# Kernel tuning notes

Measured on AMD Instinct MI355X. Metric: run time of the kernel, lower is better.

## Reference

```python
import jax, jax.numpy as jnp
import numpy as np

N_NODES = 100000
N_EDGES = 1600000
D_IN = 128
D_OUT = 128
N_RATES = 5


def setup_inputs() -> dict:
    key = jax.random.key(0)
    k1, k2, k3, k4, k5 = jax.random.split(key, 5)
    h = jax.random.normal(k1, (N_NODES, D_IN), dtype=jnp.float32)
    W = jax.random.normal(k2, (N_RATES, D_IN, D_OUT), dtype=jnp.float32) / np.sqrt(D_IN)
    b = jnp.zeros((N_RATES, D_OUT), dtype=jnp.float32)
    src = jax.random.randint(k3, (N_EDGES,), 0, N_NODES, dtype=jnp.int64)
    dst = jax.random.randint(k4, (N_EDGES,), 0, N_NODES, dtype=jnp.int64)
    rate = jax.random.randint(k5, (N_EDGES,), 0, N_RATES, dtype=jnp.int64)
    return {"h": h, "W": W, "b": b, "src": src, "dst": dst, "rate": rate}


def reference(h, W, b, src, dst, rate):
    # Per-rate edge-masked GraphConv (dgl GraphConv, norm='both'), outputs concatenated.
    # Edge subgraph is expressed as a 0/1 edge weight so shapes stay static under jit.
    N = h.shape[0]
    outs = []
    for r in range(W.shape[0]):  # small fixed set of relation types
        w_e = (rate == r).astype(h.dtype)                      # [E] subgraph mask
        out_deg = jax.ops.segment_sum(w_e, src, num_segments=N)
        in_deg = jax.ops.segment_sum(w_e, dst, num_segments=N)
        norm_src = jnp.maximum(out_deg, 1.0) ** -0.5           # dgl clamps deg to >=1
        norm_dst = jnp.maximum(in_deg, 1.0) ** -0.5
        feat = h * norm_src[:, None]                           # D_out^{-1/2} h
        msg = feat[src] * w_e[:, None]                         # gather + mask [E, D]
        agg = jax.ops.segment_sum(msg, dst, num_segments=N)    # SpMM aggregation
        outs.append((agg @ W[r]) * norm_dst[:, None] + b[r])   # weight, D_in^{-1/2}, bias
    return jnp.concatenate(outs, axis=1)                       # [N, N_RATES*D_OUT]
```

## Files before the change

kernel.cpp:

```cpp
#include <hip/hip_runtime.h>

#define N_NODES 100000
#define N_EDGES 1600000
#define DIM 128
#define N_RATES 5
#define OUT_W (N_RATES * DIM)
#define PK_SHIFT 17
#define PK_MASK  0x1FFFF
#define SCAN_NB ((N_NODES + 1023) / 1024)

#define WS_DEG_OUT 0x000000u
#define WS_DEG_IN  0x200000u
#define WS_NSRC    0x400000u
#define WS_NDST    0x600000u
#define WS_OFFS    0x800000u
#define WS_CURSOR  0x880000u
#define WS_BSUM    0x900000u
#define WS_PACKED  0xA00000u
#define WS_G       0x1100000u
#define SLOT_BYTES ((size_t)N_NODES * DIM * sizeof(float))

__global__ __launch_bounds__(256) void deg_kernel(const int* __restrict__ src,
                                                  const int* __restrict__ dst,
                                                  const int* __restrict__ rate,
                                                  int* __restrict__ deg_out,
                                                  int* __restrict__ deg_in) {
    int e = blockIdx.x * 256 + threadIdx.x;
    if (e >= N_EDGES) return;
    int r = rate[e];
    atomicAdd(&deg_out[r * N_NODES + src[e]], 1);
    atomicAdd(&deg_in [r * N_NODES + dst[e]], 1);
}

__global__ __launch_bounds__(256) void norm_kernel(const int* __restrict__ deg_out,
                                                   const int* __restrict__ deg_in,
                                                   float* __restrict__ nsrc,
                                                   float* __restrict__ ndst) {
    int i = blockIdx.x * 256 + threadIdx.x;
    if (i >= N_RATES * N_NODES) return;
    int d0 = deg_out[i]; if (d0 < 1) d0 = 1;
    int d1 = deg_in[i];  if (d1 < 1) d1 = 1;
    nsrc[i] = 1.0f / sqrtf((float)d0);
    ndst[i] = 1.0f / sqrtf((float)d1);
}

__global__ __launch_bounds__(256) void scan1_kernel(const int* __restrict__ deg_in,
                                                    int* __restrict__ offs,
                                                    int* __restrict__ bsum) {
    __shared__ int sh[256];
    int tid = threadIdx.x;
    int base = blockIdx.x * 1024 + tid * 4;
    int v[4];
#pragma unroll
    for (int j = 0; j < 4; ++j) {
        int idx = base + j, s = 0;
        if (idx < N_NODES) {
#pragma unroll
            for (int r = 0; r < N_RATES; ++r) s += deg_in[r * N_NODES + idx];
        }
        v[j] = s;
    }
    int tsum = v[0] + v[1] + v[2] + v[3];
    sh[tid] = tsum;
    __syncthreads();
    for (int off = 1; off < 256; off <<= 1) {
        int t = (tid >= off) ? sh[tid - off] : 0;
        __syncthreads();
        sh[tid] += t;
        __syncthreads();
    }
    int excl = sh[tid] - tsum;
#pragma unroll
    for (int j = 0; j < 4; ++j) {
        int idx = base + j;
        if (idx < N_NODES) offs[idx] = excl;
        excl += v[j];
    }
    if (tid == 255) bsum[blockIdx.x] = sh[255];
}

__global__ void scan2_kernel(int* __restrict__ bsum) {
    if (threadIdx.x != 0 || blockIdx.x != 0) return;
    int run = 0;
    for (int i = 0; i < SCAN_NB; ++i) { int t = bsum[i]; bsum[i] = run; run += t; }
}

__global__ __launch_bounds__(256) void scan3_kernel(int* __restrict__ offs,
                                                    const int* __restrict__ bsum,
                                                    int* __restrict__ cursor) {
    int i = blockIdx.x * 256 + threadIdx.x;
    if (i >= N_NODES) return;
    int v = offs[i] + bsum[i >> 10];
    offs[i] = v;
    cursor[i] = v;
}

__global__ __launch_bounds__(256) void fill_kernel(const int* __restrict__ src,
                                                   const int* __restrict__ dst,
                                                   const int* __restrict__ rate,
                                                   int* __restrict__ cursor,
                                                   int* __restrict__ packed) {
    int e = blockIdx.x * 256 + threadIdx.x;
    if (e >= N_EDGES) return;
    int pos = atomicAdd(&cursor[dst[e]], 1);
    packed[pos] = src[e] | (rate[e] << PK_SHIFT);
}

__global__ __launch_bounds__(256) void gemm_g_kernel(const float* __restrict__ h,
                                                     const float* __restrict__ Wall,
                                                     const float* __restrict__ nsrc,
                                                     float* __restrict__ G,
                                                     int rbase) {
    __shared__ float sW[32][128];
    __shared__ float sA[32][64];
    int slot = blockIdx.y;
    int r = rbase + slot;
    const float* W  = Wall + (size_t)r * DIM * DIM;
    const float* ns = nsrc + (size_t)r * N_NODES;
    int tid  = threadIdx.x;
    int row0 = blockIdx.x * 64;
    int c2   = (tid & 63) * 2;
    int rg   = tid >> 6;
    int rb   = rg * 16;

    float acc0[16], acc1[16];
#pragma unroll
    for (int i = 0; i < 16; ++i) { acc0[i] = 0.f; acc1[i] = 0.f; }

    for (int kc = 0; kc < 128; kc += 32) {
        __syncthreads();
#pragma unroll
        for (int j = 0; j < 4; ++j) {
            int f = tid * 4 + j * 1024;
            int kl = f >> 7, c = f & 127;
            *(float4*)(&sW[kl][c]) = *(const float4*)(W + (kc + kl) * 128 + c);
        }
#pragma unroll
        for (int j = 0; j < 2; ++j) {
            int f = tid * 4 + j * 1024;
            int rowl = f >> 5, kl = f & 31;
            int grow = row0 + rowl;
            float4 a4 = make_float4(0.f, 0.f, 0.f, 0.f);
            if (grow < N_NODES) a4 = *(const float4*)(h + (size_t)grow * DIM + kc + kl);
            sA[kl + 0][rowl] = a4.x; sA[kl + 1][rowl] = a4.y;
            sA[kl + 2][rowl] = a4.z; sA[kl + 3][rowl] = a4.w;
        }
        __syncthreads();
#pragma unroll
        for (int k = 0; k < 32; ++k) {
            float2 w = *(const float2*)(&sW[k][c2]);
#pragma unroll
            for (int i = 0; i < 4; ++i) {
                float4 a = *(const float4*)(&sA[k][rb + i * 4]);
                acc0[i*4+0] += a.x * w.x; acc1[i*4+0] += a.x * w.y;
                acc0[i*4+1] += a.y * w.x; acc1[i*4+1] += a.y * w.y;
                acc0[i*4+2] += a.z * w.x; acc1[i*4+2] += a.z * w.y;
                acc0[i*4+3] += a.w * w.x; acc1[i*4+3] += a.w * w.y;
            }
        }
    }
#pragma unroll
    for (int i = 0; i < 16; ++i) {
        int row = row0 + rb + i;
        if (row < N_NODES) {
            float nsv = ns[row];
            float2 o; o.x = acc0[i] * nsv; o.y = acc1[i] * nsv;
            *(float2*)(G + ((size_t)slot * N_NODES + row) * DIM + c2) = o;
        }
    }
}

template<int GS, bool ALL>
__global__ __launch_bounds__(256) void gather_kernel(const float* __restrict__ G,
                                                     const int* __restrict__ packed,
                                                     const int* __restrict__ offs,
                                                     const float* __restrict__ ndst,
                                                     const float* __restrict__ bias,
                                                     float* __restrict__ out,
                                                     int rbase) {
    int gw   = (blockIdx.x * 256 + threadIdx.x) >> 6;
    int lane = threadIdx.x & 63;
    if (gw >= N_NODES) return;
    int d = gw;
    int beg = offs[d];
    int end = (d == N_NODES - 1) ? N_EDGES : offs[d + 1];

    float2 a0 = make_float2(0.f, 0.f), a1 = a0, a2 = a0, a3 = a0, a4 = a0;

    int p = beg;
    for (; p + 4 <= end; p += 4) {
        int pk[4]; int rl[4]; bool use[4]; float2 v[4];
#pragma unroll
        for (int i = 0; i < 4; ++i) pk[i] = packed[p + i];
#pragma unroll
        for (int i = 0; i < 4; ++i) {
            rl[i]  = (pk[i] >> PK_SHIFT) - rbase;
            use[i] = ALL || ((unsigned)rl[i] < (unsigned)GS);
        }
#pragma unroll
        for (int i = 0; i < 4; ++i) {
            int s = pk[i] & PK_MASK;
            if (use[i])
                v[i] = *(const float2*)(G + ((size_t)rl[i] * N_NODES + s) * DIM + lane * 2);
        }
#pragma unroll
        for (int i = 0; i < 4; ++i) {
            if (!use[i]) continue;
            switch (rl[i]) {
                case 0: a0.x += v[i].x; a0.y += v[i].y; break;
                case 1: if constexpr (GS > 1) { a1.x += v[i].x; a1.y += v[i].y; } break;
                case 2: if constexpr (GS > 2) { a2.x += v[i].x; a2.y += v[i].y; } break;
                case 3: if constexpr (GS > 3) { a3.x += v[i].x; a3.y += v[i].y; } break;
                default: if constexpr (GS > 4) { a4.x += v[i].x; a4.y += v[i].y; } break;
            }
        }
    }
    for (; p < end; ++p) {
        int pkx = packed[p];
        int rlx = (pkx >> PK_SHIFT) - rbase;
        if (!ALL && (unsigned)rlx >= (unsigned)GS) continue;
        int s = pkx & PK_MASK;
        float2 v = *(const float2*)(G + ((size_t)rlx * N_NODES + s) * DIM + lane * 2);
        switch (rlx) {
            case 0: a0.x += v.x; a0.y += v.y; break;
            case 1: if constexpr (GS > 1) { a1.x += v.x; a1.y += v.y; } break;
            case 2: if constexpr (GS > 2) { a2.x += v.x; a2.y += v.y; } break;
            case 3: if constexpr (GS > 3) { a3.x += v.x; a3.y += v.y; } break;
            default: if constexpr (GS > 4) { a4.x += v.x; a4.y += v.y; } break;
        }
    }

    float* orow = out + (size_t)d * OUT_W + lane * 2;
#pragma unroll
    for (int ri = 0; ri < GS; ++ri) {
        int r = rbase + ri;
        float ndv = ndst[(size_t)r * N_NODES + d];
        float2 bb = *(const float2*)(bias + r * DIM + lane * 2);
        float2 acc = (ri == 0) ? a0 : (ri == 1) ? a1 : (ri == 2) ? a2
                   : (ri == 3) ? a3 : a4;
        float2 o; o.x = acc.x * ndv + bb.x; o.y = acc.y * ndv + bb.y;
        *(float2*)(orow + r * DIM) = o;
    }
}

__global__ __launch_bounds__(256) void zero_out_kernel(float4* __restrict__ out) {
    int i = blockIdx.x * 256 + threadIdx.x;
    if (i < N_NODES * OUT_W / 4) out[i] = make_float4(0.f, 0.f, 0.f, 0.f);
}

__global__ __launch_bounds__(256) void scatter_c_kernel(const float* __restrict__ h,
                                                        const int* __restrict__ src,
                                                        const int* __restrict__ dst,
                                                        const int* __restrict__ rate,
                                                        const float* __restrict__ nsrc,
                                                        float* __restrict__ out) {
    int lane = threadIdx.x & 63;
    int gw = (blockIdx.x * 256 + threadIdx.x) >> 6;
    int e0 = gw * 4;
#pragma unroll
    for (int i = 0; i < 4; ++i) {
        int e = e0 + i;
        if (e >= N_EDGES) return;
        int s = src[e], d = dst[e], r = rate[e];
        float ns = nsrc[(size_t)r * N_NODES + s];
        float2 v = *(const float2*)(h + (size_t)s * DIM + lane * 2);
        float* o = out + (size_t)d * OUT_W + r * DIM + lane * 2;
        unsafeAtomicAdd(o,     v.x * ns);
        unsafeAtomicAdd(o + 1, v.y * ns);
    }
}

__global__ __launch_bounds__(256) void gemm_inplace_kernel(float* __restrict__ outp,
                                                           const float* __restrict__ Wall,
                                                           const float* __restrict__ bias,
                                                           const float* __restrict__ ndst,
                                                           int r) {
    __shared__ float sW[32][128];
    __shared__ float sA[32][64];
    float* A = outp + r * DIM;
    const float* Wr = Wall + (size_t)r * DIM * DIM;
    const float* nd = ndst + (size_t)r * N_NODES;
    const float* br = bias + (size_t)r * DIM;
    int tid  = threadIdx.x;
    int row0 = blockIdx.x * 64;
    int c2   = (tid & 63) * 2;
    int rg   = tid >> 6;
    int rb   = rg * 16;
    float acc0[16], acc1[16];
#pragma unroll
    for (int i = 0; i < 16; ++i) { acc0[i] = 0.f; acc1[i] = 0.f; }
    for (int kc = 0; kc < 128; kc += 32) {
        __syncthreads();
#pragma unroll
        for (int j = 0; j < 4; ++j) {
            int f = tid * 4 + j * 1024;
            int kl = f >> 7, c = f & 127;
            *(float4*)(&sW[kl][c]) = *(const float4*)(Wr + (kc + kl) * 128 + c);
        }
#pragma unroll
        for (int j = 0; j < 2; ++j) {
            int f = tid * 4 + j * 1024;
            int rowl = f >> 5, kl = f & 31;
            int grow = row0 + rowl;
            float4 a4 = make_float4(0.f, 0.f, 0.f, 0.f);
            if (grow < N_NODES) a4 = *(const float4*)(A + (size_t)grow * OUT_W + kc + kl);
            sA[kl + 0][rowl] = a4.x; sA[kl + 1][rowl] = a4.y;
            sA[kl + 2][rowl] = a4.z; sA[kl + 3][rowl] = a4.w;
        }
        __syncthreads();
#pragma unroll
        for (int k = 0; k < 32; ++k) {
            float2 w = *(const float2*)(&sW[k][c2]);
#pragma unroll
            for (int i = 0; i < 4; ++i) {
                float4 a = *(const float4*)(&sA[k][rb + i * 4]);
                acc0[i*4+0] += a.x * w.x; acc1[i*4+0] += a.x * w.y;
                acc0[i*4+1] += a.y * w.x; acc1[i*4+1] += a.y * w.y;
                acc0[i*4+2] += a.z * w.x; acc1[i*4+2] += a.z * w.y;
                acc0[i*4+3] += a.w * w.x; acc1[i*4+3] += a.w * w.y;
            }
        }
    }
#pragma unroll
    for (int i = 0; i < 16; ++i) {
        int row = row0 + rb + i;
        if (row < N_NODES) {
            float ndv = nd[row];
            float2 o;
            o.x = acc0[i] * ndv + br[c2];
            o.y = acc1[i] * ndv + br[c2 + 1];
            *(float2*)(A + (size_t)row * OUT_W + c2) = o;
        }
    }
}

extern "C" void kernel_launch(void* const* d_in, const int* in_sizes, int n_in,
                              void* d_out, int out_size, void* d_ws, size_t ws_size,
                              hipStream_t stream) {
    const float* h    = (const float*)d_in[0];
    const float* W    = (const float*)d_in[1];
    const float* b    = (const float*)d_in[2];
    const int*   src  = (const int*)d_in[3];
    const int*   dst  = (const int*)d_in[4];
    const int*   rate = (const int*)d_in[5];
    float* out = (float*)d_out;

    char* ws = (char*)d_ws;
    int*   deg_out = (int*)(ws + WS_DEG_OUT);
    int*   deg_in  = (int*)(ws + WS_DEG_IN);
    float* nsrc    = (float*)(ws + WS_NSRC);
    float* ndst    = (float*)(ws + WS_NDST);
    int*   offs    = (int*)(ws + WS_OFFS);
    int*   cursor  = (int*)(ws + WS_CURSOR);
    int*   bsum    = (int*)(ws + WS_BSUM);
    int*   packed  = (int*)(ws + WS_PACKED);
    float* G       = (float*)(ws + WS_G);

    int n_slots = 0;
    if (ws_size > WS_G) n_slots = (int)((ws_size - WS_G) / SLOT_BYTES);
    if (n_slots > N_RATES) n_slots = N_RATES;

    hipMemsetAsync(ws, 0, 0x400000, stream);
    deg_kernel<<<(N_EDGES + 255) / 256, 256, 0, stream>>>(src, dst, rate, deg_out, deg_in);
    norm_kernel<<<(N_RATES * N_NODES + 255) / 256, 256, 0, stream>>>(deg_out, deg_in,
                                                                     nsrc, ndst);

    if (n_slots >= 1) {
        scan1_kernel<<<SCAN_NB, 256, 0, stream>>>(deg_in, offs, bsum);
        scan2_kernel<<<1, 1, 0, stream>>>(bsum);
        scan3_kernel<<<(N_NODES + 255) / 256, 256, 0, stream>>>(offs, bsum, cursor);
        fill_kernel<<<(N_EDGES + 255) / 256, 256, 0, stream>>>(src, dst, rate,
                                                               cursor, packed);
        const int ggrid = (N_NODES * 64 + 255) / 256;
        int done = 0;
        while (done < N_RATES) {
            int gs = N_RATES - done; if (gs > n_slots) gs = n_slots;
            gemm_g_kernel<<<dim3((N_NODES + 63) / 64, gs), 256, 0, stream>>>(h, W, nsrc,
                                                                             G, done);
            switch (gs) {
                case 5: gather_kernel<5, true ><<<ggrid, 256, 0, stream>>>(G, packed, offs,
                                                                           ndst, b, out, done); break;
                case 4: gather_kernel<4, false><<<ggrid, 256, 0, stream>>>(G, packed, offs,
                                                                           ndst, b, out, done); break;
                case 3: gather_kernel<3, false><<<ggrid, 256, 0, stream>>>(G, packed, offs,
                                                                           ndst, b, out, done); break;
                case 2: gather_kernel<2, false><<<ggrid, 256, 0, stream>>>(G, packed, offs,
                                                                           ndst, b, out, done); break;
                default: gather_kernel<1, false><<<ggrid, 256, 0, stream>>>(G, packed, offs,
                                                                            ndst, b, out, done); break;
            }
            done += gs;
        }
    } else {
        zero_out_kernel<<<(N_NODES * OUT_W / 4 + 255) / 256, 256, 0, stream>>>((float4*)out);
        scatter_c_kernel<<<(N_EDGES / 4 * 64 + 255) / 256, 256, 0, stream>>>(h, src, dst,
                                                                             rate, nsrc, out);
        for (int r = 0; r < N_RATES; ++r)
            gemm_inplace_kernel<<<(N_NODES + 63) / 64, 256, 0, stream>>>(out, W, b, ndst, r);
    }
}
```

Baseline: 948.1 us.

## Aggregate raw features first, then apply weights with split-bf16 MFMA GEMM

Reorders the computation so the gather aggregates source-normalized h directly, applying nsrc per edge, instead of gathering a precomputed h·W per rate. The per-rate aggregates are stored as hi/lo bf16 pairs and multiplied by W using a new MFMA kernel with three-term split-bf16 products to approximate fp32 accuracy. This removes the large fp32 G materialization. The gather now reads a single shared h table instead of five rate-specific tables, improving cache reuse, at the cost of an extra per-edge nsrc load and a bf16 intermediate round trip.

```diff
diff --git a/kernel.cpp b/kernel.cpp
--- a/kernel.cpp
+++ b/kernel.cpp
@@ -1,4 +1,5 @@
 #include <hip/hip_runtime.h>
+#include <hip/hip_bf16.h>
 
 #define N_NODES 100000
 #define N_EDGES 1600000
@@ -8,6 +9,7 @@
 #define PK_SHIFT 17
 #define PK_MASK  0x1FFFF
 #define SCAN_NB ((N_NODES + 1023) / 1024)
+#define MT_TILES ((N_NODES + 63) / 64)
 
 #define WS_DEG_OUT 0x000000u
 #define WS_DEG_IN  0x200000u
@@ -18,7 +20,10 @@
 #define WS_BSUM    0x900000u
 #define WS_PACKED  0xA00000u
 #define WS_G       0x1100000u
-#define SLOT_BYTES ((size_t)N_NODES * DIM * sizeof(float))
+#define SLOT_BYTES ((size_t)N_NODES * 256 * sizeof(unsigned short))
+
+typedef float f4     __attribute__((ext_vector_type(4)));
+typedef short bf16x8 __attribute__((ext_vector_type(8)));
 
 __global__ __launch_bounds__(256) void deg_kernel(const int* __restrict__ src,
                                                   const int* __restrict__ dst,
@@ -106,82 +111,17 @@
     packed[pos] = src[e] | (rate[e] << PK_SHIFT);
 }
 
-__global__ __launch_bounds__(256) void gemm_g_kernel(const float* __restrict__ h,
-                                                     const float* __restrict__ Wall,
-                                                     const float* __restrict__ nsrc,
-                                                     float* __restrict__ G,
-                                                     int rbase) {
-    __shared__ float sW[32][128];
-    __shared__ float sA[32][64];
-    int slot = blockIdx.y;
-    int r = rbase + slot;
-    const float* W  = Wall + (size_t)r * DIM * DIM;
-    const float* ns = nsrc + (size_t)r * N_NODES;
-    int tid  = threadIdx.x;
-    int row0 = blockIdx.x * 64;
-    int c2   = (tid & 63) * 2;
-    int rg   = tid >> 6;
-    int rb   = rg * 16;
-
-    float acc0[16], acc1[16];
-#pragma unroll
-    for (int i = 0; i < 16; ++i) { acc0[i] = 0.f; acc1[i] = 0.f; }
-
-    for (int kc = 0; kc < 128; kc += 32) {
-        __syncthreads();
-#pragma unroll
-        for (int j = 0; j < 4; ++j) {
-            int f = tid * 4 + j * 1024;
-            int kl = f >> 7, c = f & 127;
-            *(float4*)(&sW[kl][c]) = *(const float4*)(W + (kc + kl) * 128 + c);
-        }
-#pragma unroll
-        for (int j = 0; j < 2; ++j) {
-            int f = tid * 4 + j * 1024;
-            int rowl = f >> 5, kl = f & 31;
-            int grow = row0 + rowl;
-            float4 a4 = make_float4(0.f, 0.f, 0.f, 0.f);
-            if (grow < N_NODES) a4 = *(const float4*)(h + (size_t)grow * DIM + kc + kl);
-            sA[kl + 0][rowl] = a4.x; sA[kl + 1][rowl] = a4.y;
-            sA[kl + 2][rowl] = a4.z; sA[kl + 3][rowl] = a4.w;
-        }
-        __syncthreads();
-#pragma unroll
-        for (int k = 0; k < 32; ++k) {
-            float2 w = *(const float2*)(&sW[k][c2]);
-#pragma unroll
-            for (int i = 0; i < 4; ++i) {
-                float4 a = *(const float4*)(&sA[k][rb + i * 4]);
-                acc0[i*4+0] += a.x * w.x; acc1[i*4+0] += a.x * w.y;
-                acc0[i*4+1] += a.y * w.x; acc1[i*4+1] += a.y * w.y;
-                acc0[i*4+2] += a.z * w.x; acc1[i*4+2] += a.z * w.y;
-                acc0[i*4+3] += a.w * w.x; acc1[i*4+3] += a.w * w.y;
-            }
-        }
-    }
-#pragma unroll
-    for (int i = 0; i < 16; ++i) {
-        int row = row0 + rb + i;
-        if (row < N_NODES) {
-            float nsv = ns[row];
-            float2 o; o.x = acc0[i] * nsv; o.y = acc1[i] * nsv;
-            *(float2*)(G + ((size_t)slot * N_NODES + row) * DIM + c2) = o;
-        }
-    }
-}
-
 template<int GS, bool ALL>
-__global__ __launch_bounds__(256) void gather_kernel(const float* __restrict__ G,
+__global__ __launch_bounds__(256) void gather_kernel(const float* __restrict__ h,
                                                      const int* __restrict__ packed,
                                                      const int* __restrict__ offs,
-                                                     const float* __restrict__ ndst,
-                                                     const float* __restrict__ bias,
-                                                     float* __restrict__ out,
+                                                     const float* __restrict__ nsrc,
+                                                     unsigned short* __restrict__ agg,
                                                      int rbase) {
     int gw   = (blockIdx.x * 256 + threadIdx.x) >> 6;
     int lane = threadIdx.x & 63;
     if (gw >= N_NODES) return;
-    int d = gw;
+    const int d = gw;
     int beg = offs[d];
     int end = (d == N_NODES - 1) ? N_EDGES : offs[d + 1];
 
@@ -189,7 +129,7 @@
 
     int p = beg;
     for (; p + 4 <= end; p += 4) {
-        int pk[4]; int rl[4]; bool use[4]; float2 v[4];
+        int pk[4]; int rl[4]; bool use[4]; float2 v[4]; float ns[4];
 #pragma unroll
         for (int i = 0; i < 4; ++i) pk[i] = packed[p + i];
 #pragma unroll
@@ -200,18 +140,21 @@
 #pragma unroll
         for (int i = 0; i < 4; ++i) {
             int s = pk[i] & PK_MASK;
-            if (use[i])
-                v[i] = *(const float2*)(G + ((size_t)rl[i] * N_NODES + s) * DIM + lane * 2);
+            if (use[i]) {
+                v[i]  = *(const float2*)(h + (size_t)s * DIM + lane * 2);
+                ns[i] = nsrc[(size_t)(rl[i] + rbase) * N_NODES + s];
+            }
         }
 #pragma unroll
         for (int i = 0; i < 4; ++i) {
             if (!use[i]) continue;
+            float tx = v[i].x * ns[i], ty = v[i].y * ns[i];
             switch (rl[i]) {
-                case 0: a0.x += v[i].x; a0.y += v[i].y; break;
-                case 1: if constexpr (GS > 1) { a1.x += v[i].x; a1.y += v[i].y; } break;
-                case 2: if constexpr (GS > 2) { a2.x += v[i].x; a2.y += v[i].y; } break;
-                case 3: if constexpr (GS > 3) { a3.x += v[i].x; a3.y += v[i].y; } break;
-                default: if constexpr (GS > 4) { a4.x += v[i].x; a4.y += v[i].y; } break;
+                case 0: a0.x += tx; a0.y += ty; break;
+                case 1: if constexpr (GS > 1) { a1.x += tx; a1.y += ty; } break;
+                case 2: if constexpr (GS > 2) { a2.x += tx; a2.y += ty; } break;
+                case 3: if constexpr (GS > 3) { a3.x += tx; a3.y += ty; } break;
+                default: if constexpr (GS > 4) { a4.x += tx; a4.y += ty; } break;
             }
         }
     }
@@ -220,26 +163,107 @@
         int rlx = (pkx >> PK_SHIFT) - rbase;
         if (!ALL && (unsigned)rlx >= (unsigned)GS) continue;
         int s = pkx & PK_MASK;
-        float2 v = *(const float2*)(G + ((size_t)rlx * N_NODES + s) * DIM + lane * 2);
+        float2 v = *(const float2*)(h + (size_t)s * DIM + lane * 2);
+        float ns = nsrc[(size_t)(rlx + rbase) * N_NODES + s];
+        float tx = v.x * ns, ty = v.y * ns;
         switch (rlx) {
-            case 0: a0.x += v.x; a0.y += v.y; break;
-            case 1: if constexpr (GS > 1) { a1.x += v.x; a1.y += v.y; } break;
-            case 2: if constexpr (GS > 2) { a2.x += v.x; a2.y += v.y; } break;
-            case 3: if constexpr (GS > 3) { a3.x += v.x; a3.y += v.y; } break;
-            default: if constexpr (GS > 4) { a4.x += v.x; a4.y += v.y; } break;
-        }
-    }
-
-    float* orow = out + (size_t)d * OUT_W + lane * 2;
+            case 0: a0.x += tx; a0.y += ty; break;
+            case 1: if constexpr (GS > 1) { a1.x += tx; a1.y += ty; } break;
+            case 2: if constexpr (GS > 2) { a2.x += tx; a2.y += ty; } break;
+            case 3: if constexpr (GS > 3) { a3.x += tx; a3.y += ty; } break;
+            default: if constexpr (GS > 4) { a4.x += tx; a4.y += ty; } break;
+        }
+    }
+
 #pragma unroll
     for (int ri = 0; ri < GS; ++ri) {
-        int r = rbase + ri;
-        float ndv = ndst[(size_t)r * N_NODES + d];
-        float2 bb = *(const float2*)(bias + r * DIM + lane * 2);
         float2 acc = (ri == 0) ? a0 : (ri == 1) ? a1 : (ri == 2) ? a2
                    : (ri == 3) ? a3 : a4;
-        float2 o; o.x = acc.x * ndv + bb.x; o.y = acc.y * ndv + bb.y;
-        *(float2*)(orow + r * DIM) = o;
+        unsigned short* row = agg + ((size_t)ri * N_NODES + d) * 256;
+        __bf16 hx = (__bf16)acc.x; __bf16 lx = (__bf16)(acc.x - (float)hx);
+        __bf16 hy = (__bf16)acc.y; __bf16 ly = (__bf16)(acc.y - (float)hy);
+        unsigned int hv = (unsigned int)__builtin_bit_cast(unsigned short, hx)
+                        | ((unsigned int)__builtin_bit_cast(unsigned short, hy) << 16);
+        unsigned int lv = (unsigned int)__builtin_bit_cast(unsigned short, lx)
+                        | ((unsigned int)__builtin_bit_cast(unsigned short, ly) << 16);
+        *(unsigned int*)(row + lane * 2)       = hv;
+        *(unsigned int*)(row + 128 + lane * 2) = lv;
+    }
+}
+
+__global__ __launch_bounds__(256) void gemm_agg_kernel(const unsigned short* __restrict__ agg,
+                                                       const float* __restrict__ Wall,
+                                                       const float* __restrict__ bias,
+                                                       const float* __restrict__ ndst,
+                                                       float* __restrict__ out,
+                                                       int rbase) {
+    __shared__ __align__(16) unsigned short sWt[2][128][136];
+    const int slot = blockIdx.y;
+    const int r = rbase + slot;
+    const float* Wr = Wall + (size_t)r * DIM * DIM;
+    const int tid = threadIdx.x;
+
+#pragma unroll
+    for (int phase = 0; phase < 16; ++phase) {
+        int f = phase * 1024 + tid * 4;
+        int k = f >> 7, n = f & 127;
+        float4 w4 = *(const float4*)(Wr + f);
+        float wv[4] = {w4.x, w4.y, w4.z, w4.w};
+#pragma unroll
+        for (int j = 0; j < 4; ++j) {
+            __bf16 hb = (__bf16)wv[j];
+            __bf16 lb = (__bf16)(wv[j] - (float)hb);
+            sWt[0][n + j][k] = __builtin_bit_cast(unsigned short, hb);
+            sWt[1][n + j][k] = __builtin_bit_cast(unsigned short, lb);
+        }
+    }
+    __syncthreads();
+
+    const int w = tid >> 6, l = tid & 63;
+    const int lrow = l & 15;
+    const int lk   = (l >> 4) * 8;
+    const int lq4  = (l >> 4) * 4;
+    const float* ndr = ndst + (size_t)r * N_NODES;
+    const float* br  = bias + (size_t)r * DIM;
+
+    for (int mt = blockIdx.x; mt < MT_TILES; mt += gridDim.x) {
+        int rowA = mt * 64 + w * 16 + lrow;
+        int rowAc = rowA < N_NODES ? rowA : 0;
+        const unsigned short* arow = agg + ((size_t)slot * N_NODES + rowAc) * 256;
+
+        f4 acc[8];
+#pragma unroll
+        for (int i = 0; i < 8; ++i) acc[i] = (f4){0.f, 0.f, 0.f, 0.f};
+
+#pragma unroll
+        for (int ks = 0; ks < 4; ++ks) {
+            int k0 = ks * 32;
+            bf16x8 ah = *(const bf16x8*)(arow + k0 + lk);
+            bf16x8 al = *(const bf16x8*)(arow + 128 + k0 + lk);
+#pragma unroll
+            for (int nt = 0; nt < 8; ++nt) {
+                bf16x8 bh = *(const bf16x8*)&sWt[0][nt * 16 + lrow][k0 + lk];
+                bf16x8 bl = *(const bf16x8*)&sWt[1][nt * 16 + lrow][k0 + lk];
+                acc[nt] = __builtin_amdgcn_mfma_f32_16x16x32_bf16(ah, bh, acc[nt], 0, 0, 0);
+                acc[nt] = __builtin_amdgcn_mfma_f32_16x16x32_bf16(ah, bl, acc[nt], 0, 0, 0);
+                acc[nt] = __builtin_amdgcn_mfma_f32_16x16x32_bf16(al, bh, acc[nt], 0, 0, 0);
+            }
+        }
+
+        int rowD0 = mt * 64 + w * 16 + lq4;
+#pragma unroll
+        for (int q = 0; q < 4; ++q) {
+            int row = rowD0 + q;
+            if (row < N_NODES) {
+                float ndv = ndr[row];
+                float* orow = out + (size_t)row * OUT_W + r * DIM;
+#pragma unroll
+                for (int nt = 0; nt < 8; ++nt) {
+                    int col = nt * 16 + lrow;
+                    orow[col] = acc[nt][q] * ndv + br[col];
+                }
+            }
+        }
     }
 }
 
@@ -310,14 +334,14 @@
         __syncthreads();
 #pragma unroll
         for (int k = 0; k < 32; ++k) {
-            float2 w = *(const float2*)(&sW[k][c2]);
+            float2 wv = *(const float2*)(&sW[k][c2]);
 #pragma unroll
             for (int i = 0; i < 4; ++i) {
                 float4 a = *(const float4*)(&sA[k][rb + i * 4]);
-                acc0[i*4+0] += a.x * w.x; acc1[i*4+0] += a.x * w.y;
-                acc0[i*4+1] += a.y * w.x; acc1[i*4+1] += a.y * w.y;
-                acc0[i*4+2] += a.z * w.x; acc1[i*4+2] += a.z * w.y;
-                acc0[i*4+3] += a.w * w.x; acc1[i*4+3] += a.w * w.y;
+                acc0[i*4+0] += a.x * wv.x; acc1[i*4+0] += a.x * wv.y;
+                acc0[i*4+1] += a.y * wv.x; acc1[i*4+1] += a.y * wv.y;
+                acc0[i*4+2] += a.z * wv.x; acc1[i*4+2] += a.z * wv.y;
+                acc0[i*4+3] += a.w * wv.x; acc1[i*4+3] += a.w * wv.y;
             }
         }
     }
@@ -354,7 +378,7 @@
     int*   cursor  = (int*)(ws + WS_CURSOR);
     int*   bsum    = (int*)(ws + WS_BSUM);
     int*   packed  = (int*)(ws + WS_PACKED);
-    float* G       = (float*)(ws + WS_G);
+    unsigned short* agg = (unsigned short*)(ws + WS_G);
 
     int n_slots = 0;
     if (ws_size > WS_G) n_slots = (int)((ws_size - WS_G) / SLOT_BYTES);
@@ -375,20 +399,19 @@
         int done = 0;
         while (done < N_RATES) {
             int gs = N_RATES - done; if (gs > n_slots) gs = n_slots;
-            gemm_g_kernel<<<dim3((N_NODES + 63) / 64, gs), 256, 0, stream>>>(h, W, nsrc,
-                                                                             G, done);
             switch (gs) {
-                case 5: gather_kernel<5, true ><<<ggrid, 256, 0, stream>>>(G, packed, offs,
-                                                                           ndst, b, out, done); break;
-                case 4: gather_kernel<4, false><<<ggrid, 256, 0, stream>>>(G, packed, offs,
-                                                                           ndst, b, out, done); break;
-                case 3: gather_kernel<3, false><<<ggrid, 256, 0, stream>>>(G, packed, offs,
-                                                                           ndst, b, out, done); break;
-                case 2: gather_kernel<2, false><<<ggrid, 256, 0, stream>>>(G, packed, offs,
-                                                                           ndst, b, out, done); break;
-                default: gather_kernel<1, false><<<ggrid, 256, 0, stream>>>(G, packed, offs,
-                                                                            ndst, b, out, done); break;
-            }
+                case 5: gather_kernel<5, true ><<<ggrid, 256, 0, stream>>>(h, packed, offs,
+                                                                           nsrc, agg, done); break;
+                case 4: gather_kernel<4, false><<<ggrid, 256, 0, stream>>>(h, packed, offs,
+                                                                           nsrc, agg, done); break;
+                case 3: gather_kernel<3, false><<<ggrid, 256, 0, stream>>>(h, packed, offs,
+                                                                           nsrc, agg, done); break;
+                case 2: gather_kernel<2, false><<<ggrid, 256, 0, stream>>>(h, packed, offs,
+                                                                           nsrc, agg, done); break;
+                default: gather_kernel<1, false><<<ggrid, 256, 0, stream>>>(h, packed, offs,
+                                                                            nsrc, agg, done); break;
+            }
+            gemm_agg_kernel<<<dim3(256, gs), 256, 0, stream>>>(agg, W, b, ndst, out, done);
             done += gs;
         }
     } else {
```

New measurement: 965.3 us. Within noise of the previous version (+1.8%).
